# Optimization experiments

Measured on AMD Instinct MI355X. Metric: run time of the kernel, lower is better.

The kernel has to match this reference:

```python
import jax, jax.numpy as jnp
import numpy as np

T, N, E = 8, 50000, 800000
XD, HD, GD, ZD, TD, YHD = 128, 256, 128, 128, 8, 16
PSH = 100          # ps_predictor hidden width
BN_EPS = 1e-5


def _dense(k, fan_in, shape):
    return jax.random.normal(k, shape, jnp.float32) * (1.0 / np.sqrt(fan_in))


def setup_inputs() -> dict:
    ks = jax.random.split(jax.random.key(0), 20)
    inp = {}
    inp["X"] = jax.random.normal(ks[0], (T, N, XD), jnp.float32)
    inp["C"] = jax.random.uniform(ks[1], (T, N, TD), dtype=jnp.float32)
    inp["Y_hist"] = jax.random.normal(ks[2], (T, N, YHD), jnp.float32)
    inp["edge_index"] = jax.random.randint(ks[3], (T, 2, E), 0, N)
    # parameters
    inp["phi_W"] = _dense(ks[4], XD, (XD, HD)); inp["phi_b"] = jnp.zeros((HD,), jnp.float32)
    inp["gc_W"] = _dense(ks[5], HD, (T, HD, GD)); inp["gc_b"] = jnp.zeros((T, GD), jnp.float32)
    inp["ew_logit"] = jax.random.normal(ks[6], (T, E), jnp.float32) * 0.1  # learned edge weights (pre-sigmoid)
    inp["fuse_W"] = _dense(ks[7], 2 * HD + GD, (2 * HD + GD, ZD)); inp["fuse_b"] = jnp.zeros((ZD,), jnp.float32)
    inp["o00_W"] = _dense(ks[8], ZD, (ZD, ZD)); inp["o00_b"] = jnp.zeros((ZD,), jnp.float32)
    inp["o10_W"] = _dense(ks[9], ZD, (ZD, ZD)); inp["o10_b"] = jnp.zeros((ZD,), jnp.float32)
    inp["o01_W"] = _dense(ks[10], ZD, (ZD, 1)); inp["o01_b"] = jnp.zeros((1,), jnp.float32)
    inp["o11_W"] = _dense(ks[11], ZD, (ZD, 1)); inp["o11_b"] = jnp.zeros((1,), jnp.float32)
    inp["ps1_W"] = _dense(ks[12], ZD, (ZD, PSH)); inp["ps1_b"] = jnp.zeros((PSH,), jnp.float32)
    inp["bn_g"] = jnp.ones((PSH,), jnp.float32); inp["bn_b"] = jnp.zeros((PSH,), jnp.float32)
    inp["ps2_W"] = _dense(ks[13], PSH, (PSH, 2)); inp["ps2_b"] = jnp.zeros((2,), jnp.float32)
    inp["gru_Wih"] = _dense(ks[14], ZD + TD + YHD, (3 * HD, ZD + TD + YHD))
    inp["gru_Whh"] = _dense(ks[15], HD, (3 * HD, HD))
    inp["gru_bih"] = jnp.zeros((3 * HD,), jnp.float32)
    inp["gru_bhh"] = jnp.zeros((3 * HD,), jnp.float32)
    return inp


def reference(X, C, Y_hist, edge_index, phi_W, phi_b, gc_W, gc_b, ew_logit,
              fuse_W, fuse_b, o00_W, o00_b, o10_W, o10_b, o01_W, o01_b,
              o11_W, o11_b, ps1_W, ps1_b, bn_g, bn_b, ps2_W, ps2_b,
              gru_Wih, gru_Whh, gru_bih, gru_bhh):
    h0 = jnp.zeros((N, HD), X.dtype)
    bn_scale = bn_g / jnp.sqrt(1.0 + BN_EPS)  # eval-mode BN: running_mean=0, running_var=1

    def step(h, xs):
        x, ei, c, yh, W_t, b_t, ewl_t = xs
        phi = jax.nn.relu(x @ phi_W + phi_b)                              # [N,HD]
        # --- GCNConv with learned sigmoid edge weights + self loops ---
        src, dst = ei[0], ei[1]
        ew = jax.nn.sigmoid(ewl_t)                                        # [E]
        deg = jax.ops.segment_sum(ew, dst, num_segments=N) + 1.0          # +1 for self-loop weight
        dinv = jax.lax.rsqrt(deg)
        norm = dinv[src] * ew * dinv[dst]                                 # symmetric norm per edge
        xw = phi @ W_t                                                    # [N,GD]
        agg = jax.ops.segment_sum(norm[:, None] * xw[src], dst, num_segments=N)
        agg = agg + xw / deg[:, None] + b_t                               # self-loop contribution + bias
        rep = jax.nn.relu(agg)                                            # [N,GD] (dropout off in eval)
        # --- fuse with skip connection ---
        z = jax.nn.relu(jnp.concatenate([h, rep, phi], axis=1) @ fuse_W + fuse_b)  # [N,ZD]
        # --- GRUCell (torch gate order: reset, update, new) ---
        inp = jnp.concatenate([z, c, yh], axis=1)
        gi = inp @ gru_Wih.T + gru_bih
        gh = h @ gru_Whh.T + gru_bhh
        i_r, i_z, i_n = jnp.split(gi, 3, axis=1)
        h_r, h_z, h_n = jnp.split(gh, 3, axis=1)
        r = jax.nn.sigmoid(i_r + h_r)
        u = jax.nn.sigmoid(i_z + h_z)
        n = jnp.tanh(i_n + r * h_n)
        h_new = (1.0 - u) * n + u * h
        # --- outcome heads ---
        y0 = jax.nn.relu(z @ o00_W + o00_b) @ o01_W + o01_b               # [N,1]
        y1 = jax.nn.relu(z @ o10_W + o10_b) @ o11_W + o11_b               # [N,1]
        # --- propensity head (BatchNorm eval, sigmoid, softmax) ---
        s = jax.nn.sigmoid((z @ ps1_W + ps1_b) * bn_scale + bn_b)
        ps = jax.nn.softmax(s @ ps2_W + ps2_b, axis=1)                    # [N,2]
        return h_new, (y1, y0, z, ps)

    h_fin, (all_y1, all_y0, all_z, all_ps) = jax.lax.scan(
        step, h0, (X, edge_index, C, Y_hist, gc_W, gc_b, ew_logit))
    return all_y1, all_y0, all_z, all_ps, h_fin
```

## Files before the change

### kernel.cpp

```cpp
#include <hip/hip_runtime.h>
#include <math.h>

#define T_STEPS 8
#define NN 50000
#define EE 800000
#define TN (T_STEPS*NN)
#define TE (T_STEPS*EE)

typedef unsigned int uint;
typedef unsigned short ushort;
typedef unsigned long long u64;
typedef __attribute__((ext_vector_type(8))) short short8;
typedef __attribute__((ext_vector_type(4))) float f32x4;

__device__ __forceinline__ float sigf(float x){ return 1.0f/(1.0f+expf(-x)); }
__device__ __forceinline__ ushort f2b(float f){
  uint x = __float_as_uint(f);
  uint r = (x + 0x7fffu + ((x>>16)&1u)) >> 16;
  return (ushort)r;
}
__device__ __forceinline__ float b2f(ushort u){ return __uint_as_float(((uint)u)<<16); }

__device__ __forceinline__ void gload16(const ushort* g, ushort* l){
  __builtin_amdgcn_global_load_lds(
      (const __attribute__((address_space(1))) void*)g,
      (__attribute__((address_space(3))) void*)l, 16, 0, 0);
}

template<int ROWS>
__device__ __forceinline__ void stage_tile(const ushort* base, int ld, int rowclamp,
                                           ushort* lds, int lane, int wid){
  constexpr int ITERS = ROWS/32;
#pragma unroll
  for (int i=0;i<ITERS;i++){
    int lin = i*256 + wid*64 + lane;
    int row = lin>>3, s = lin&7;
    int gr = row; if (gr > rowclamp) gr = rowclamp;
    const ushort* gp = base + (size_t)gr*ld + ((s ^ (row&7))<<3);
    gload16(gp, lds + (size_t)(i*256 + wid*64)*8);
  }
}

__device__ __forceinline__ short8 fragld(const ushort* lds, int R, int kk, int lane){
  int slot = (kk*4 + (lane>>4)) ^ (R&7);
  return *(const short8*)&lds[R*64 + slot*8];
}

__global__ __launch_bounds__(256,2) void gemm_bf(
    const ushort* __restrict__ A0, int ld0, int w0,
    const ushort* __restrict__ A1, int ld1,
    const ushort* __restrict__ W, int K2,
    const float* __restrict__ bias, int act,
    float* __restrict__ C32, int ldc,
    ushort* __restrict__ C16, int ldb,
    int Nrow, int NOvalid)
{
  __shared__ __align__(16) ushort As[8192];
  __shared__ __align__(16) ushort Bs[8192];
  const int tid  = threadIdx.x;
  const int lane = tid & 63;
  const int wid  = __builtin_amdgcn_readfirstlane(tid >> 6);
  const int brow = blockIdx.x*128;
  const int bcol = blockIdx.y*128;
  const int wr = wid>>1, wc = wid&1;

  f32x4 acc[4][4];
#pragma unroll
  for(int m=0;m<4;m++)
#pragma unroll
    for(int n=0;n<4;n++) acc[m][n] = (f32x4){0.f,0.f,0.f,0.f};

  const int nk = K2 >> 6;
  for (int kt=0; kt<nk; ++kt){
    int col0 = kt*64;
    const ushort* ab; int ald;
    if (col0 < w0){ ab = A0 + col0; ald = ld0; }
    else          { ab = A1 + (col0 - w0); ald = ld1; }
    stage_tile<128>(ab + (size_t)brow*ald, ald, Nrow-1-brow, As, lane, wid);
    stage_tile<128>(W + (size_t)bcol*K2 + col0, K2, 1<<30, Bs, lane, wid);
    __syncthreads();
#pragma unroll
    for (int kk=0;kk<2;kk++){
      short8 a[4], b[4];
#pragma unroll
      for (int m=0;m<4;m++) a[m] = fragld(As, wr*64 + m*16 + (lane&15), kk, lane);
#pragma unroll
      for (int n=0;n<4;n++) b[n] = fragld(Bs, wc*64 + n*16 + (lane&15), kk, lane);
#pragma unroll
      for (int m=0;m<4;m++)
#pragma unroll
        for (int n=0;n<4;n++)
          acc[m][n] = __builtin_amdgcn_mfma_f32_16x16x32_bf16(a[m], b[n], acc[m][n], 0,0,0);
    }
    __syncthreads();
  }
  const int rbase = brow + wr*64 + (lane>>4)*4;
  const int cbase = bcol + wc*64 + (lane&15);
#pragma unroll
  for (int m=0;m<4;m++){
#pragma unroll
    for (int q=0;q<4;q++){
      int r = rbase + m*16 + q;
      if (r >= Nrow) continue;
#pragma unroll
      for (int n=0;n<4;n++){
        int c = cbase + n*16;
        if (c >= NOvalid) continue;
        float v = acc[m][n][q];
        if (bias)  v += bias[c];
        if (act==1) v = fmaxf(v, 0.f);
        if (C32) C32[(size_t)r*ldc + c] = v;
        if (C16) C16[(size_t)r*ldb + c] = f2b(v);
      }
    }
  }
}

__global__ __launch_bounds__(256,2) void gemm_gru(
    const ushort* __restrict__ A0, int ld0, int w0,
    const ushort* __restrict__ A1, int ld1,
    const ushort* __restrict__ W,
    const float* __restrict__ bg,
    const float* __restrict__ hin,
    float* __restrict__ hout, ushort* __restrict__ hbfo,
    int Nrow)
{
  __shared__ __align__(16) ushort As[8192];
  __shared__ __align__(16) ushort Bs[8192];
  const int tid  = threadIdx.x;
  const int lane = tid & 63;
  const int wid  = __builtin_amdgcn_readfirstlane(tid >> 6);
  const int brow = blockIdx.x*128;
  const int bcol = blockIdx.y*128;
  const int wr = wid>>1, wc = wid&1;
  const int K2 = 448;

  f32x4 acc[4][4];
#pragma unroll
  for(int m=0;m<4;m++)
#pragma unroll
    for(int n=0;n<4;n++) acc[m][n] = (f32x4){0.f,0.f,0.f,0.f};

  for (int kt=0; kt<7; ++kt){
    int col0 = kt*64;
    const ushort* ab; int ald;
    if (col0 < w0){ ab = A0 + col0; ald = ld0; }
    else          { ab = A1 + (col0 - w0); ald = ld1; }
    stage_tile<128>(ab + (size_t)brow*ald, ald, Nrow-1-brow, As, lane, wid);
    stage_tile<128>(W + (size_t)bcol*K2 + col0, K2, 1<<30, Bs, lane, wid);
    __syncthreads();
#pragma unroll
    for (int kk=0;kk<2;kk++){
      short8 a[4], b[4];
#pragma unroll
      for (int m=0;m<4;m++) a[m] = fragld(As, wr*64 + m*16 + (lane&15), kk, lane);
#pragma unroll
      for (int n=0;n<4;n++) b[n] = fragld(Bs, wc*64 + n*16 + (lane&15), kk, lane);
#pragma unroll
      for (int m=0;m<4;m++)
#pragma unroll
        for (int n=0;n<4;n++)
          acc[m][n] = __builtin_amdgcn_mfma_f32_16x16x32_bf16(a[m], b[n], acc[m][n], 0,0,0);
    }
    __syncthreads();
  }
  const int jj = lane&15;
  const int j  = blockIdx.y*32 + wc*16 + jj;
  const int rbase = brow + wr*64 + (lane>>4)*4;
  float bb[4];
#pragma unroll
  for (int n=0;n<4;n++) bb[n] = bg[bcol + wc*64 + n*16 + jj];
#pragma unroll
  for (int m=0;m<4;m++){
#pragma unroll
    for (int q=0;q<4;q++){
      int r = rbase + m*16 + q;
      if (r >= Nrow) continue;
      float v0 = acc[m][0][q] + bb[0];
      float v1 = acc[m][1][q] + bb[1];
      float v2 = acc[m][2][q] + bb[2];
      float v3 = acc[m][3][q] + bb[3];
      float rg = sigf(v0), ug = sigf(v1);
      float ng = tanhf(v2 + rg*v3);
      float ho = hin[(size_t)r*256 + j];
      float hn = (1.f-ug)*ng + ug*ho;
      hout[(size_t)r*256 + j] = hn;
      hbfo[(size_t)r*256 + j] = f2b(hn);
    }
  }
}

__global__ __launch_bounds__(256,2) void heads_k(
    const ushort* __restrict__ A, int ldA,
    const ushort* __restrict__ W,
    const float* __restrict__ o00b, const float* __restrict__ o10b,
    const float* __restrict__ w01, const float* __restrict__ b01,
    const float* __restrict__ w11, const float* __restrict__ b11,
    float* __restrict__ y0out, float* __restrict__ y1out, int Nrow)
{
  __shared__ __align__(16) ushort As[4096];
  __shared__ __align__(16) ushort Bs[16384];
  __shared__ float shy[4][64];
  const int tid  = threadIdx.x;
  const int lane = tid & 63;
  const int wid  = __builtin_amdgcn_readfirstlane(tid >> 6);
  const int brow = blockIdx.x*64;

  f32x4 acc[4][4];
#pragma unroll
  for(int m=0;m<4;m++)
#pragma unroll
    for(int n=0;n<4;n++) acc[m][n] = (f32x4){0.f,0.f,0.f,0.f};

  for (int kt=0; kt<2; ++kt){
    stage_tile<64>(A + (size_t)brow*ldA + kt*64, ldA, Nrow-1-brow, As, lane, wid);
    stage_tile<256>(W + kt*64, 128, 1<<30, Bs, lane, wid);
    __syncthreads();
#pragma unroll
    for (int kk=0;kk<2;kk++){
      short8 a[4], b[4];
#pragma unroll
      for (int m=0;m<4;m++) a[m] = fragld(As, m*16 + (lane&15), kk, lane);
#pragma unroll
      for (int n=0;n<4;n++) b[n] = fragld(Bs, wid*64 + n*16 + (lane&15), kk, lane);
#pragma unroll
      for (int m=0;m<4;m++)
#pragma unroll
        for (int n=0;n<4;n++)
          acc[m][n] = __builtin_amdgcn_mfma_f32_16x16x32_bf16(a[m], b[n], acc[m][n], 0,0,0);
    }
    __syncthreads();
  }
  float bb[4], ww[4];
#pragma unroll
  for (int n=0;n<4;n++){
    int c = wid*64 + n*16 + (lane&15);
    bb[n] = (c<128)? o00b[c] : o10b[c-128];
    ww[n] = (c<128)? w01[c]  : w11[c-128];
  }
#pragma unroll
  for (int m=0;m<4;m++){
#pragma unroll
    for (int q=0;q<4;q++){
      float p = 0.f;
#pragma unroll
      for (int n=0;n<4;n++) p += fmaxf(acc[m][n][q] + bb[n], 0.f) * ww[n];
#pragma unroll
      for (int o=1;o<16;o<<=1) p += __shfl_xor(p, o);
      if ((lane&15)==0) shy[wid][m*16 + (lane>>4)*4 + q] = p;
    }
  }
  __syncthreads();
  if (tid < 64){
    int r = brow + tid;
    if (r < Nrow){
      y0out[r] = shy[0][tid] + shy[1][tid] + b01[0];
      y1out[r] = shy[2][tid] + shy[3][tid] + b11[0];
    }
  }
}

__global__ __launch_bounds__(256,2) void ps_k(
    const ushort* __restrict__ A, int ldA,
    const ushort* __restrict__ W,
    const float* __restrict__ psc, const float* __restrict__ psb,
    const float* __restrict__ W2, const float* __restrict__ b2,
    float* __restrict__ psout, int Nrow)
{
  __shared__ __align__(16) ushort As[8192];
  __shared__ __align__(16) ushort Bs[8192];
  __shared__ float sh0[2][128];
  __shared__ float sh1[2][128];
  const int tid  = threadIdx.x;
  const int lane = tid & 63;
  const int wid  = __builtin_amdgcn_readfirstlane(tid >> 6);
  const int brow = blockIdx.x*128;
  const int wr = wid>>1, wc = wid&1;

  f32x4 acc[4][4];
#pragma unroll
  for(int m=0;m<4;m++)
#pragma unroll
    for(int n=0;n<4;n++) acc[m][n] = (f32x4){0.f,0.f,0.f,0.f};

  for (int kt=0; kt<2; ++kt){
    stage_tile<128>(A + (size_t)brow*ldA + kt*64, ldA, Nrow-1-brow, As, lane, wid);
    stage_tile<128>(W + kt*64, 128, 1<<30, Bs, lane, wid);
    __syncthreads();
#pragma unroll
    for (int kk=0;kk<2;kk++){
      short8 a[4], b[4];
#pragma unroll
      for (int m=0;m<4;m++) a[m] = fragld(As, wr*64 + m*16 + (lane&15), kk, lane);
#pragma unroll
      for (int n=0;n<4;n++) b[n] = fragld(Bs, wc*64 + n*16 + (lane&15), kk, lane);
#pragma unroll
      for (int m=0;m<4;m++)
#pragma unroll
        for (int n=0;n<4;n++)
          acc[m][n] = __builtin_amdgcn_mfma_f32_16x16x32_bf16(a[m], b[n], acc[m][n], 0,0,0);
    }
    __syncthreads();
  }
  float sc[4], sb[4], w0_[4], w1_[4];
#pragma unroll
  for (int n=0;n<4;n++){
    int c = wc*64 + n*16 + (lane&15);
    bool ok = (c<100);
    sc[n] = ok? psc[c] : 0.f;
    sb[n] = ok? psb[c] : 0.f;
    w0_[n]= ok? W2[2*c] : 0.f;
    w1_[n]= ok? W2[2*c+1] : 0.f;
  }
#pragma unroll
  for (int m=0;m<4;m++){
#pragma unroll
    for (int q=0;q<4;q++){
      float a0=0.f, a1=0.f;
#pragma unroll
      for (int n=0;n<4;n++){
        float s = sigf(acc[m][n][q]*sc[n] + sb[n]);
        a0 += s*w0_[n]; a1 += s*w1_[n];
      }
#pragma unroll
      for (int o=1;o<16;o<<=1){ a0 += __shfl_xor(a0,o); a1 += __shfl_xor(a1,o); }
      if ((lane&15)==0){
        int rt = wr*64 + m*16 + (lane>>4)*4 + q;
        sh0[wc][rt] = a0; sh1[wc][rt] = a1;
      }
    }
  }
  __syncthreads();
  if (tid < 128){
    int r = brow + tid;
    if (r < Nrow){
      float l0 = sh0[0][tid]+sh0[1][tid]+b2[0];
      float l1 = sh1[0][tid]+sh1[1][tid]+b2[1];
      float mx = fmaxf(l0,l1);
      float e0 = expf(l0-mx), e1 = expf(l1-mx);
      float inv = 1.f/(e0+e1);
      psout[(size_t)r*2]   = e0*inv;
      psout[(size_t)r*2+1] = e1*inv;
    }
  }
}

__global__ void count_k(const int* __restrict__ ei, const float* __restrict__ ewl,
                        u64* __restrict__ degcnt)
{
  int idx = blockIdx.x*256 + threadIdx.x;
  if (idx >= TE) return;
  int t = idx / EE;
  int e = idx - t*EE;
  const int* dst = ei + (size_t)t*2*EE + EE;
  int d = dst[e];
  u64 v = (1ULL<<40) | (u64)(uint)(sigf(ewl[idx]) * 1048576.0f);
  atomicAdd((unsigned long long*)&degcnt[t*NN + d], (unsigned long long)v);
}

__global__ void dinv_k(const u64* __restrict__ degcnt, int* __restrict__ cnt,
                       float* __restrict__ dnv, float* __restrict__ invd){
  int idx = blockIdx.x*256+threadIdx.x;
  if (idx>=TN) return;
  u64 tot = degcnt[idx];
  int c = (int)(tot>>40);
  float S = (float)(tot & ((1ULL<<40)-1)) * (1.f/1048576.f);
  float dv = S + 1.f;
  cnt[idx] = c;
  dnv[idx]  = rsqrtf(dv);
  invd[idx] = 1.f/dv;
}

__global__ void scan1_k(const int* __restrict__ in, int* __restrict__ outv,
                        int* __restrict__ partials, int n)
{
  __shared__ int sh[256];
  int base = blockIdx.x*1024;
  int tid = threadIdx.x;
  int v[4]; int s=0;
#pragma unroll
  for (int i=0;i<4;i++){ int idx=base+tid*4+i; v[i] = (idx<n)? in[idx]:0; s+=v[i]; }
  sh[tid]=s; __syncthreads();
  for (int o=1;o<256;o<<=1){
    int t2 = (tid>=o)? sh[tid-o]:0;
    __syncthreads();
    sh[tid]+=t2;
    __syncthreads();
  }
  int excl = sh[tid]-s;
#pragma unroll
  for (int i=0;i<4;i++){ int idx=base+tid*4+i; if(idx<n) outv[idx]=excl; excl+=v[i]; }
  if (tid==255) partials[blockIdx.x]=sh[255];
}

__global__ void scan2_k(int* p, int np){
  __shared__ int sh[256];
  __shared__ int run;
  int tid=threadIdx.x;
  if(tid==0) run=0;
  __syncthreads();
  for(int base=0;base<np;base+=256){
    int v = (base+tid<np)? p[base+tid]:0;
    sh[tid]=v; __syncthreads();
    for(int o=1;o<256;o<<=1){
      int t2 = (tid>=o)? sh[tid-o]:0;
      __syncthreads();
      sh[tid]+=t2;
      __syncthreads();
    }
    int incl=sh[tid];
    int r0=run;
    __syncthreads();
    if(base+tid<np) p[base+tid]=r0+incl-v;
    __syncthreads();
    if(tid==0) run = r0 + sh[255];
    __syncthreads();
  }
}

__global__ void scan3_k(int* __restrict__ offs, const int* __restrict__ parts,
                        int* __restrict__ cur, int n){
  int idx = blockIdx.x*256+threadIdx.x;
  if (idx==0) offs[n] = TE;
  if (idx<n){ int v = offs[idx] + parts[idx>>10]; offs[idx]=v; cur[idx]=v; }
}

__global__ void fill_k(const int* __restrict__ ei, const float* __restrict__ ewl,
                       const float* __restrict__ dnv, int* __restrict__ cur,
                       u64* __restrict__ epack)
{
  int idx = blockIdx.x*256 + threadIdx.x;
  if (idx >= TE) return;
  int t = idx / EE;
  int e = idx - t*EE;
  const int* srcp = ei + (size_t)t*2*EE;
  const int* dstp = srcp + EE;
  int s=srcp[e], d=dstp[e];
  float nr = dnv[t*NN+s] * sigf(ewl[idx]) * dnv[t*NN+d];
  int pos = atomicAdd(&cur[t*NN+d], 1);
  epack[pos] = (u64)(uint)s | ((u64)__float_as_uint(nr) << 32);
}

__global__ __launch_bounds__(256) void gather_k(const int* __restrict__ offs_t,
    const u64* __restrict__ epack,
    const ushort* __restrict__ xwb, const float* __restrict__ invd_t,
    const float* __restrict__ gcb_t, ushort* __restrict__ rp)
{
  int node = blockIdx.x*4 + (threadIdx.x>>6);
  int lane = threadIdx.x & 63;
  if (node >= NN) return;
  int o0 = offs_t[node], o1 = offs_t[node+1];
  float a0=0.f, a1=0.f;
  int j=o0;
  for (; j+1<o1; j+=2){
    u64 e0 = epack[j], e1 = epack[j+1];
    uint r0 = ((const uint*)(xwb + ((size_t)(uint)e0)*128))[lane];
    uint r1 = ((const uint*)(xwb + ((size_t)(uint)e1)*128))[lane];
    float n0 = __uint_as_float((uint)(e0>>32));
    float n1 = __uint_as_float((uint)(e1>>32));
    a0 = fmaf(n0, b2f((ushort)(r0&0xffff)), a0);
    a1 = fmaf(n0, b2f((ushort)(r0>>16)),   a1);
    a0 = fmaf(n1, b2f((ushort)(r1&0xffff)), a0);
    a1 = fmaf(n1, b2f((ushort)(r1>>16)),   a1);
  }
  if (j<o1){
    u64 e0 = epack[j];
    uint r0 = ((const uint*)(xwb + ((size_t)(uint)e0)*128))[lane];
    float n0 = __uint_as_float((uint)(e0>>32));
    a0 = fmaf(n0, b2f((ushort)(r0&0xffff)), a0);
    a1 = fmaf(n0, b2f((ushort)(r0>>16)),   a1);
  }
  float sl = invd_t[node];
  uint us = ((const uint*)(xwb + (size_t)node*128))[lane];
  a0 = fmaf(sl, b2f((ushort)(us&0xffff)), a0) + gcb_t[2*lane];
  a1 = fmaf(sl, b2f((ushort)(us>>16)),   a1) + gcb_t[2*lane+1];
  a0 = fmaxf(a0, 0.f); a1 = fmaxf(a1, 0.f);
  uint pk = (uint)f2b(a0) | ((uint)f2b(a1) << 16);
  ((uint*)(rp + (size_t)node*384))[lane] = pk;
}

__global__ void convT_k(ushort* __restrict__ dst, const float* __restrict__ src,
                        int O, int Osrc, int K, int Kp)
{
  int idx = blockIdx.x*256 + threadIdx.x;
  if (idx >= O*Kp) return;
  dst += (size_t)blockIdx.y * O * Kp;
  src += (size_t)blockIdx.y * K * Osrc;
  int o = idx / Kp, k = idx - o*Kp;
  float v = (k<K && o<Osrc) ? src[(size_t)k*Osrc + o] : 0.f;
  dst[idx] = f2b(v);
}

__global__ void woc_k(ushort* __restrict__ dst, const float* __restrict__ o00W,
                      const float* __restrict__ o10W)
{
  int idx = blockIdx.x*256 + threadIdx.x;
  if (idx >= 256*128) return;
  int o = idx >> 7, k = idx & 127;
  float v = (o<128) ? o00W[(size_t)k*128 + o] : o10W[(size_t)k*128 + (o-128)];
  dst[idx] = f2b(v);
}

__global__ void wgru_k(const float* __restrict__ Wih, const float* __restrict__ Whh,
                       const float* __restrict__ bih, const float* __restrict__ bhh,
                       ushort* __restrict__ Wg, float* __restrict__ bg)
{
  int idx = blockIdx.x*256 + threadIdx.x;
  if (idx >= 1024*448) return;
  int c = idx/448, k = idx - c*448;
  int G = c>>6, g = (c>>4)&3, jj = c&15;
  int j = G*16 + jj;
  float v = 0.f;
  if (k < 152){
    if      (g==0) v = Wih[(size_t)j*152 + k];
    else if (g==1) v = Wih[(size_t)(256+j)*152 + k];
    else if (g==2) v = Wih[(size_t)(512+j)*152 + k];
  } else if (k >= 192){
    int kk = k-192;
    if      (g==0) v = Whh[(size_t)j*256 + kk];
    else if (g==1) v = Whh[(size_t)(256+j)*256 + kk];
    else if (g==3) v = Whh[(size_t)(512+j)*256 + kk];
  }
  Wg[idx] = f2b(v);
  if (k==0){
    float b;
    if      (g==0) b = bih[j]     + bhh[j];
    else if (g==1) b = bih[256+j] + bhh[256+j];
    else if (g==2) b = bih[512+j];
    else           b = bhh[512+j];
    bg[c] = b;
  }
}

__global__ void misc_k(const float* __restrict__ ps1b, const float* __restrict__ bng,
                       const float* __restrict__ bnb,
                       float* __restrict__ psc, float* __restrict__ psb)
{
  int i = threadIdx.x;
  if (i<100){ float sc = bng[i]*rsqrtf(1.f+1e-5f); psc[i]=sc; psb[i]=ps1b[i]*sc+bnb[i]; }
  else if (i<128){ psc[i]=0.f; psb[i]=0.f; }
}

__global__ void xconv_k(ushort* __restrict__ dst, const float* __restrict__ src, long n4)
{
  long i = (long)blockIdx.x*256 + threadIdx.x;
  if (i >= n4) return;
  float4 v = ((const float4*)src)[i];
  uint lo = (uint)f2b(v.x) | ((uint)f2b(v.y)<<16);
  uint hi = (uint)f2b(v.z) | ((uint)f2b(v.w)<<16);
  ((uint2*)dst)[i] = make_uint2(lo, hi);
}

__global__ void cyh_k(ushort* __restrict__ zcyh, const float* __restrict__ Cc,
                      const float* __restrict__ Yh)
{
  int gid = blockIdx.x*256 + threadIdx.x;
  int n = gid >> 6, l = gid & 63;
  if (n >= NN) return;
  float v = 0.f;
  if (l < 8)       v = Cc[(size_t)n*8 + l];
  else if (l < 24) v = Yh[(size_t)n*16 + (l-8)];
  zcyh[(size_t)n*192 + 128 + l] = f2b(v);
}

extern "C" void kernel_launch(void* const* d_in, const int* in_sizes, int n_in,
                              void* d_out_v, int out_size, void* d_ws, size_t ws_size,
                              hipStream_t stream)
{
  const float* X    = (const float*)d_in[0];
  const float* Cc   = (const float*)d_in[1];
  const float* Yh   = (const float*)d_in[2];
  const int*   EI   = (const int*)  d_in[3];
  const float* phiW = (const float*)d_in[4];  const float* phib = (const float*)d_in[5];
  const float* gcW  = (const float*)d_in[6];  const float* gcb  = (const float*)d_in[7];
  const float* ewl  = (const float*)d_in[8];
  const float* fuseW= (const float*)d_in[9];  const float* fuseb= (const float*)d_in[10];
  const float* o00W = (const float*)d_in[11]; const float* o00b = (const float*)d_in[12];
  const float* o10W = (const float*)d_in[13]; const float* o10b = (const float*)d_in[14];
  const float* o01W = (const float*)d_in[15]; const float* o01b = (const float*)d_in[16];
  const float* o11W = (const float*)d_in[17]; const float* o11b = (const float*)d_in[18];
  const float* ps1W = (const float*)d_in[19]; const float* ps1b = (const float*)d_in[20];
  const float* bng  = (const float*)d_in[21]; const float* bnb  = (const float*)d_in[22];
  const float* ps2W = (const float*)d_in[23]; const float* ps2b = (const float*)d_in[24];
  const float* Wih  = (const float*)d_in[25]; const float* Whh  = (const float*)d_in[26];
  const float* bih  = (const float*)d_in[27]; const float* bhh  = (const float*)d_in[28];
  float* out = (float*)d_out_v;

  char* wsb = (char*)d_ws;
  size_t off=0;
  auto alloc=[&](size_t bytes)->void*{
    void* p = wsb + off;
    off = (off + bytes + 255) & ~(size_t)255;
    return p;
  };
  u64*   degcnt= (u64*)  alloc((size_t)TN*8);
  int*   cnt   = (int*)  alloc((size_t)TN*4);
  int*   cur   = (int*)  alloc((size_t)TN*4);
  int*   offs  = (int*)  alloc(((size_t)TN+1)*4);
  float* dnv   = (float*)alloc((size_t)TN*4);
  float* invd  = (float*)alloc((size_t)TN*4);
  u64*   epack = (u64*)  alloc((size_t)TE*8);
  int*   parts = (int*)  alloc(4096);
  ushort* Xb   = (ushort*)alloc((size_t)T_STEPS*NN*128*2);
  ushort* rp   = (ushort*)alloc((size_t)NN*384*2);
  ushort* zcyh = (ushort*)alloc((size_t)NN*192*2);
  ushort* xwb  = (ushort*)alloc((size_t)NN*128*2);
  ushort* hbf0 = (ushort*)alloc((size_t)NN*256*2);
  ushort* hbf1 = (ushort*)alloc((size_t)NN*256*2);
  float* hb0   = (float*)alloc((size_t)NN*256*4);
  float* hb1   = (float*)alloc((size_t)NN*256*4);
  ushort* phiWt= (ushort*)alloc(256*128*2);
  ushort* gcWt = (ushort*)alloc((size_t)T_STEPS*128*256*2);
  ushort* fuseWt=(ushort*)alloc(128*640*2);
  ushort* Wgru = (ushort*)alloc((size_t)1024*448*2);
  float* bgru  = (float*)alloc(1024*4);
  ushort* wocT = (ushort*)alloc(256*128*2);
  ushort* ps1T = (ushort*)alloc(128*128*2);
  float* psc   = (float*)alloc(128*4);
  float* psb   = (float*)alloc(128*4);

  hipMemsetAsync(degcnt, 0, (size_t)TN*8, stream);
  hipMemsetAsync(hb0,  0, (size_t)NN*256*4, stream);
  hipMemsetAsync(hbf0, 0, (size_t)NN*256*2, stream);

  misc_k<<<1,256,0,stream>>>(ps1b,bng,bnb,psc,psb);
  convT_k<<<dim3((256*128+255)/256,1),256,0,stream>>>(phiWt, phiW, 256,256,128,128);
  convT_k<<<dim3((128*256+255)/256,T_STEPS),256,0,stream>>>(gcWt, gcW, 128,128,256,256);
  convT_k<<<dim3((128*640+255)/256,1),256,0,stream>>>(fuseWt, fuseW, 128,128,640,640);
  convT_k<<<dim3((128*128+255)/256,1),256,0,stream>>>(ps1T, ps1W, 128,100,128,128);
  wgru_k<<<(1024*448+255)/256,256,0,stream>>>(Wih,Whh,bih,bhh,Wgru,bgru);
  woc_k<<<(256*128+255)/256,256,0,stream>>>(wocT, o00W, o10W);
  xconv_k<<<(int)(((size_t)T_STEPS*NN*128/4+255)/256),256,0,stream>>>(Xb, X, (long)T_STEPS*NN*128/4);

  count_k<<<(TE+255)/256,256,0,stream>>>(EI,ewl,degcnt);
  dinv_k<<<(TN+255)/256,256,0,stream>>>(degcnt,cnt,dnv,invd);
  scan1_k<<<(TN+1023)/1024,256,0,stream>>>(cnt,offs,parts,TN);
  scan2_k<<<1,256,0,stream>>>(parts,(TN+1023)/1024);
  scan3_k<<<(TN+255)/256,256,0,stream>>>(offs,parts,cur,TN);
  fill_k<<<(TE+255)/256,256,0,stream>>>(EI,ewl,dnv,cur,epack);

  const size_t zoff  = (size_t)2*TN;
  const size_t psoff = zoff + (size_t)TN*128;
  const size_t hoff  = psoff + (size_t)TN*2;
  constexpr int GX = (NN+127)/128;

  for (int t=0;t<T_STEPS;t++){
    const float*  hin  = (t&1)? hb1 : hb0;
    float*        hout = (t==T_STEPS-1)? (out+hoff) : ((t&1)? hb0 : hb1);
    const ushort* hbi  = (t&1)? hbf1 : hbf0;
    ushort*       hbo  = (t&1)? hbf0 : hbf1;
    float* zt = out + zoff + (size_t)t*NN*128;

    cyh_k<<<(NN*64+255)/256,256,0,stream>>>(zcyh, Cc+(size_t)t*NN*8, Yh+(size_t)t*NN*16);

    gemm_bf<<<dim3(GX,2),256,0,stream>>>(Xb+(size_t)t*NN*128,128,128, nullptr,0,
      phiWt,128, phib,1, nullptr,0, rp+128,384, NN,256);
    gemm_bf<<<dim3(GX,1),256,0,stream>>>(rp+128,384,256, nullptr,0,
      gcWt+(size_t)t*128*256,256, nullptr,0, nullptr,0, xwb,128, NN,128);
    gather_k<<<NN/4,256,0,stream>>>(offs+(size_t)t*NN, epack, xwb,
                                    invd+(size_t)t*NN, gcb+(size_t)t*128, rp);
    gemm_bf<<<dim3(GX,1),256,0,stream>>>(hbi,256,256, rp,384,
      fuseWt,640, fuseb,1, zt,128, zcyh,192, NN,128);
    gemm_gru<<<dim3(GX,8),256,0,stream>>>(zcyh,192,192, hbi,256,
      Wgru, bgru, hin, hout, hbo, NN);
    heads_k<<<(NN+63)/64,256,0,stream>>>(zcyh,192, wocT, o00b,o10b,
      o01W,o01b, o11W,o11b,
      out + TN + (size_t)t*NN,
      out + (size_t)t*NN, NN);
    ps_k<<<GX,256,0,stream>>>(zcyh,192, ps1T, psc,psb, ps2W,ps2b,
      out+psoff+(size_t)t*NN*2, NN);
  }
  (void)in_sizes; (void)n_in; (void)out_size; (void)ws_size;
}
```

Baseline: 2.838 ms.

## Hoist h-independent stages out of the time loop and batch them over all steps

The phi GEMM, graph-conv GEMM, gather, and the rep/phi part of the fuse GEMM now run once over all T steps, using blockIdx.z as the time index. Only the h-dependent fuse GEMM and the GRU stay in the sequential loop; the outcome heads and propensity head run batched after the loop. Edge records are packed into 32 bits (16-bit source index and 16-bit quantized weight) to halve gather traffic. The aim is to cut per-step launch overhead, fill the GPU with larger grids, and reduce memory traffic. The cost is larger workspace buffers, plus extra precision loss from the quantized edge weights and the bf16 partial fuse result.

```diff
diff --git a/kernel.cpp b/kernel.cpp
--- a/kernel.cpp
+++ b/kernel.cpp
@@ -46,17 +46,20 @@
   return *(const short8*)&lds[R*64 + slot*8];
 }
 
+struct Seg { const ushort* p; int ld; long ts; int w; };
+
 __global__ __launch_bounds__(256,2) void gemm_bf(
-    const ushort* __restrict__ A0, int ld0, int w0,
-    const ushort* __restrict__ A1, int ld1,
-    const ushort* __restrict__ W, int K2,
+    Seg s0, Seg s1, Seg s2,
+    const ushort* __restrict__ W, int K2, long Wts,
     const float* __restrict__ bias, int act,
-    float* __restrict__ C32, int ldc,
-    ushort* __restrict__ C16, int ldb,
+    const ushort* __restrict__ addp, int ldad, long adts,
+    float* __restrict__ C32, int ldc, long c32ts,
+    ushort* __restrict__ C16, int ldb, long c16ts,
     int Nrow, int NOvalid)
 {
   __shared__ __align__(16) ushort As[8192];
   __shared__ __align__(16) ushort Bs[8192];
+  const int t    = blockIdx.z;
   const int tid  = threadIdx.x;
   const int lane = tid & 63;
   const int wid  = __builtin_amdgcn_readfirstlane(tid >> 6);
@@ -74,10 +77,11 @@
   for (int kt=0; kt<nk; ++kt){
     int col0 = kt*64;
     const ushort* ab; int ald;
-    if (col0 < w0){ ab = A0 + col0; ald = ld0; }
-    else          { ab = A1 + (col0 - w0); ald = ld1; }
+    if (col0 < s0.w){ ab = s0.p + (size_t)t*s0.ts + col0; ald = s0.ld; }
+    else if (col0 < s0.w + s1.w){ ab = s1.p + (size_t)t*s1.ts + (col0 - s0.w); ald = s1.ld; }
+    else { ab = s2.p + (size_t)t*s2.ts + (col0 - s0.w - s1.w); ald = s2.ld; }
     stage_tile<128>(ab + (size_t)brow*ald, ald, Nrow-1-brow, As, lane, wid);
-    stage_tile<128>(W + (size_t)bcol*K2 + col0, K2, 1<<30, Bs, lane, wid);
+    stage_tile<128>(W + (size_t)t*Wts + (size_t)bcol*K2 + col0, K2, 1<<30, Bs, lane, wid);
     __syncthreads();
 #pragma unroll
     for (int kk=0;kk<2;kk++){
@@ -107,18 +111,18 @@
         int c = cbase + n*16;
         if (c >= NOvalid) continue;
         float v = acc[m][n][q];
-        if (bias)  v += bias[c];
+        if (addp) v += b2f(addp[(size_t)t*adts + (size_t)r*ldad + c]);
+        if (bias) v += bias[c];
         if (act==1) v = fmaxf(v, 0.f);
-        if (C32) C32[(size_t)r*ldc + c] = v;
-        if (C16) C16[(size_t)r*ldb + c] = f2b(v);
+        if (C32) C32[(size_t)t*c32ts + (size_t)r*ldc + c] = v;
+        if (C16) C16[(size_t)t*c16ts + (size_t)r*ldb + c] = f2b(v);
       }
     }
   }
 }
 
 __global__ __launch_bounds__(256,2) void gemm_gru(
-    const ushort* __restrict__ A0, int ld0, int w0,
-    const ushort* __restrict__ A1, int ld1,
+    Seg s0, Seg s1, Seg s2,
     const ushort* __restrict__ W,
     const float* __restrict__ bg,
     const float* __restrict__ hin,
@@ -144,8 +148,9 @@
   for (int kt=0; kt<7; ++kt){
     int col0 = kt*64;
     const ushort* ab; int ald;
-    if (col0 < w0){ ab = A0 + col0; ald = ld0; }
-    else          { ab = A1 + (col0 - w0); ald = ld1; }
+    if (col0 < s0.w){ ab = s0.p + col0; ald = s0.ld; }
+    else if (col0 < s0.w + s1.w){ ab = s1.p + (col0 - s0.w); ald = s1.ld; }
+    else { ab = s2.p + (col0 - s0.w - s1.w); ald = s2.ld; }
     stage_tile<128>(ab + (size_t)brow*ald, ald, Nrow-1-brow, As, lane, wid);
     stage_tile<128>(W + (size_t)bcol*K2 + col0, K2, 1<<30, Bs, lane, wid);
     __syncthreads();
@@ -167,9 +172,10 @@
   const int jj = lane&15;
   const int j  = blockIdx.y*32 + wc*16 + jj;
   const int rbase = brow + wr*64 + (lane>>4)*4;
+  const int bcolw = bcol + wc*64;
   float bb[4];
 #pragma unroll
-  for (int n=0;n<4;n++) bb[n] = bg[bcol + wc*64 + n*16 + jj];
+  for (int n=0;n<4;n++) bb[n] = bg[bcolw + n*16 + jj];
 #pragma unroll
   for (int m=0;m<4;m++){
 #pragma unroll
@@ -191,20 +197,23 @@
 }
 
 __global__ __launch_bounds__(256,2) void heads_k(
-    const ushort* __restrict__ A, int ldA,
+    const ushort* __restrict__ Az, long Ats,
     const ushort* __restrict__ W,
     const float* __restrict__ o00b, const float* __restrict__ o10b,
     const float* __restrict__ w01, const float* __restrict__ b01,
     const float* __restrict__ w11, const float* __restrict__ b11,
-    float* __restrict__ y0out, float* __restrict__ y1out, int Nrow)
+    float* __restrict__ y0out, long y0ts,
+    float* __restrict__ y1out, long y1ts, int Nrow)
 {
   __shared__ __align__(16) ushort As[4096];
   __shared__ __align__(16) ushort Bs[16384];
   __shared__ float shy[4][64];
+  const int t    = blockIdx.z;
   const int tid  = threadIdx.x;
   const int lane = tid & 63;
   const int wid  = __builtin_amdgcn_readfirstlane(tid >> 6);
   const int brow = blockIdx.x*64;
+  const ushort* A = Az + (size_t)t*Ats;
 
   f32x4 acc[4][4];
 #pragma unroll
@@ -213,7 +222,7 @@
     for(int n=0;n<4;n++) acc[m][n] = (f32x4){0.f,0.f,0.f,0.f};
 
   for (int kt=0; kt<2; ++kt){
-    stage_tile<64>(A + (size_t)brow*ldA + kt*64, ldA, Nrow-1-brow, As, lane, wid);
+    stage_tile<64>(A + (size_t)brow*128 + kt*64, 128, Nrow-1-brow, As, lane, wid);
     stage_tile<256>(W + kt*64, 128, 1<<30, Bs, lane, wid);
     __syncthreads();
 #pragma unroll
@@ -254,28 +263,30 @@
   if (tid < 64){
     int r = brow + tid;
     if (r < Nrow){
-      y0out[r] = shy[0][tid] + shy[1][tid] + b01[0];
-      y1out[r] = shy[2][tid] + shy[3][tid] + b11[0];
+      y0out[(size_t)t*y0ts + r] = shy[0][tid] + shy[1][tid] + b01[0];
+      y1out[(size_t)t*y1ts + r] = shy[2][tid] + shy[3][tid] + b11[0];
     }
   }
 }
 
 __global__ __launch_bounds__(256,2) void ps_k(
-    const ushort* __restrict__ A, int ldA,
+    const ushort* __restrict__ Az, long Ats,
     const ushort* __restrict__ W,
     const float* __restrict__ psc, const float* __restrict__ psb,
     const float* __restrict__ W2, const float* __restrict__ b2,
-    float* __restrict__ psout, int Nrow)
+    float* __restrict__ psout, long psts, int Nrow)
 {
   __shared__ __align__(16) ushort As[8192];
   __shared__ __align__(16) ushort Bs[8192];
   __shared__ float sh0[2][128];
   __shared__ float sh1[2][128];
+  const int t    = blockIdx.z;
   const int tid  = threadIdx.x;
   const int lane = tid & 63;
   const int wid  = __builtin_amdgcn_readfirstlane(tid >> 6);
   const int brow = blockIdx.x*128;
   const int wr = wid>>1, wc = wid&1;
+  const ushort* A = Az + (size_t)t*Ats;
 
   f32x4 acc[4][4];
 #pragma unroll
@@ -284,7 +295,7 @@
     for(int n=0;n<4;n++) acc[m][n] = (f32x4){0.f,0.f,0.f,0.f};
 
   for (int kt=0; kt<2; ++kt){
-    stage_tile<128>(A + (size_t)brow*ldA + kt*64, ldA, Nrow-1-brow, As, lane, wid);
+    stage_tile<128>(A + (size_t)brow*128 + kt*64, 128, Nrow-1-brow, As, lane, wid);
     stage_tile<128>(W + kt*64, 128, 1<<30, Bs, lane, wid);
     __syncthreads();
 #pragma unroll
@@ -339,8 +350,8 @@
       float mx = fmaxf(l0,l1);
       float e0 = expf(l0-mx), e1 = expf(l1-mx);
       float inv = 1.f/(e0+e1);
-      psout[(size_t)r*2]   = e0*inv;
-      psout[(size_t)r*2+1] = e1*inv;
+      psout[(size_t)t*psts + (size_t)r*2]   = e0*inv;
+      psout[(size_t)t*psts + (size_t)r*2+1] = e1*inv;
     }
   }
 }
@@ -427,7 +438,7 @@
 
 __global__ void fill_k(const int* __restrict__ ei, const float* __restrict__ ewl,
                        const float* __restrict__ dnv, int* __restrict__ cur,
-                       u64* __restrict__ epack)
+                       uint* __restrict__ epack)
 {
   int idx = blockIdx.x*256 + threadIdx.x;
   if (idx >= TE) return;
@@ -437,46 +448,51 @@
   const int* dstp = srcp + EE;
   int s=srcp[e], d=dstp[e];
   float nr = dnv[t*NN+s] * sigf(ewl[idx]) * dnv[t*NN+d];
+  uint nq = (uint)(nr*65535.f + 0.5f);
   int pos = atomicAdd(&cur[t*NN+d], 1);
-  epack[pos] = (u64)(uint)s | ((u64)__float_as_uint(nr) << 32);
-}
-
-__global__ __launch_bounds__(256) void gather_k(const int* __restrict__ offs_t,
-    const u64* __restrict__ epack,
-    const ushort* __restrict__ xwb, const float* __restrict__ invd_t,
-    const float* __restrict__ gcb_t, ushort* __restrict__ rp)
-{
+  epack[pos] = (uint)s | (nq<<16);
+}
+
+__global__ __launch_bounds__(256) void gather_k(const int* __restrict__ offs,
+    const uint* __restrict__ epack,
+    const ushort* __restrict__ xwb, const float* __restrict__ invd,
+    const float* __restrict__ gcb, ushort* __restrict__ rep)
+{
+  int t    = blockIdx.z;
   int node = blockIdx.x*4 + (threadIdx.x>>6);
   int lane = threadIdx.x & 63;
   if (node >= NN) return;
+  const int* offs_t = offs + (size_t)t*NN;
+  const ushort* xw_t = xwb + (size_t)t*NN*128;
   int o0 = offs_t[node], o1 = offs_t[node+1];
   float a0=0.f, a1=0.f;
   int j=o0;
   for (; j+1<o1; j+=2){
-    u64 e0 = epack[j], e1 = epack[j+1];
-    uint r0 = ((const uint*)(xwb + ((size_t)(uint)e0)*128))[lane];
-    uint r1 = ((const uint*)(xwb + ((size_t)(uint)e1)*128))[lane];
-    float n0 = __uint_as_float((uint)(e0>>32));
-    float n1 = __uint_as_float((uint)(e1>>32));
+    uint e0 = epack[j], e1 = epack[j+1];
+    uint r0 = ((const uint*)(xw_t + ((size_t)(e0&0xffff))*128))[lane];
+    uint r1 = ((const uint*)(xw_t + ((size_t)(e1&0xffff))*128))[lane];
+    float n0 = (float)(e0>>16) * (1.f/65535.f);
+    float n1 = (float)(e1>>16) * (1.f/65535.f);
     a0 = fmaf(n0, b2f((ushort)(r0&0xffff)), a0);
     a1 = fmaf(n0, b2f((ushort)(r0>>16)),   a1);
     a0 = fmaf(n1, b2f((ushort)(r1&0xffff)), a0);
     a1 = fmaf(n1, b2f((ushort)(r1>>16)),   a1);
   }
   if (j<o1){
-    u64 e0 = epack[j];
-    uint r0 = ((const uint*)(xwb + ((size_t)(uint)e0)*128))[lane];
-    float n0 = __uint_as_float((uint)(e0>>32));
+    uint e0 = epack[j];
+    uint r0 = ((const uint*)(xw_t + ((size_t)(e0&0xffff))*128))[lane];
+    float n0 = (float)(e0>>16) * (1.f/65535.f);
     a0 = fmaf(n0, b2f((ushort)(r0&0xffff)), a0);
     a1 = fmaf(n0, b2f((ushort)(r0>>16)),   a1);
   }
-  float sl = invd_t[node];
-  uint us = ((const uint*)(xwb + (size_t)node*128))[lane];
+  float sl = invd[(size_t)t*NN + node];
+  const float* gcb_t = gcb + (size_t)t*128;
+  uint us = ((const uint*)(xw_t + (size_t)node*128))[lane];
   a0 = fmaf(sl, b2f((ushort)(us&0xffff)), a0) + gcb_t[2*lane];
   a1 = fmaf(sl, b2f((ushort)(us>>16)),   a1) + gcb_t[2*lane+1];
   a0 = fmaxf(a0, 0.f); a1 = fmaxf(a1, 0.f);
   uint pk = (uint)f2b(a0) | ((uint)f2b(a1) << 16);
-  ((uint*)(rp + (size_t)node*384))[lane] = pk;
+  ((uint*)(rep + ((size_t)t*NN + node)*128))[lane] = pk;
 }
 
 __global__ void convT_k(ushort* __restrict__ dst, const float* __restrict__ src,
@@ -551,16 +567,16 @@
   ((uint2*)dst)[i] = make_uint2(lo, hi);
 }
 
-__global__ void cyh_k(ushort* __restrict__ zcyh, const float* __restrict__ Cc,
+__global__ void cyh_k(ushort* __restrict__ cyh, const float* __restrict__ Cc,
                       const float* __restrict__ Yh)
 {
-  int gid = blockIdx.x*256 + threadIdx.x;
-  int n = gid >> 6, l = gid & 63;
-  if (n >= NN) return;
+  long gid = (long)blockIdx.x*256 + threadIdx.x;
+  if (gid >= (long)TN*64) return;
+  long g = gid >> 6; int l = (int)(gid & 63);
   float v = 0.f;
-  if (l < 8)       v = Cc[(size_t)n*8 + l];
-  else if (l < 24) v = Yh[(size_t)n*16 + (l-8)];
-  zcyh[(size_t)n*192 + 128 + l] = f2b(v);
+  if (l < 8)       v = Cc[g*8 + l];
+  else if (l < 24) v = Yh[g*16 + (l-8)];
+  cyh[g*64 + l] = f2b(v);
 }
 
 extern "C" void kernel_launch(void* const* d_in, const int* in_sizes, int n_in,
@@ -599,19 +615,19 @@
   int*   offs  = (int*)  alloc(((size_t)TN+1)*4);
   float* dnv   = (float*)alloc((size_t)TN*4);
   float* invd  = (float*)alloc((size_t)TN*4);
-  u64*   epack = (u64*)  alloc((size_t)TE*8);
+  uint*  epack = (uint*) alloc((size_t)TE*4);
   int*   parts = (int*)  alloc(4096);
-  ushort* Xb   = (ushort*)alloc((size_t)T_STEPS*NN*128*2);
-  ushort* rp   = (ushort*)alloc((size_t)NN*384*2);
-  ushort* zcyh = (ushort*)alloc((size_t)NN*192*2);
-  ushort* xwb  = (ushort*)alloc((size_t)NN*128*2);
+  ushort* Xb   = (ushort*)alloc((size_t)TN*128*2);
+  ushort* phiA = (ushort*)alloc((size_t)TN*256*2);
+  ushort* xwb  = (ushort*)alloc((size_t)TN*128*2);
+  ushort* pz   = (ushort*)alloc((size_t)TN*128*2);
   ushort* hbf0 = (ushort*)alloc((size_t)NN*256*2);
   ushort* hbf1 = (ushort*)alloc((size_t)NN*256*2);
-  float* hb0   = (float*)alloc((size_t)NN*256*4);
-  float* hb1   = (float*)alloc((size_t)NN*256*4);
+  float*  hb   = (float*)alloc((size_t)NN*256*4);
   ushort* phiWt= (ushort*)alloc(256*128*2);
   ushort* gcWt = (ushort*)alloc((size_t)T_STEPS*128*256*2);
-  ushort* fuseWt=(ushort*)alloc(128*640*2);
+  ushort* WhT  = (ushort*)alloc(128*256*2);
+  ushort* WrpT = (ushort*)alloc(128*384*2);
   ushort* Wgru = (ushort*)alloc((size_t)1024*448*2);
   float* bgru  = (float*)alloc(1024*4);
   ushort* wocT = (ushort*)alloc(256*128*2);
@@ -619,18 +635,23 @@
   float* psc   = (float*)alloc(128*4);
   float* psb   = (float*)alloc(128*4);
 
+  ushort* rep_all = Xb;
+  ushort* zbf     = phiA;
+  ushort* cyh     = phiA + (size_t)TN*128;
+
   hipMemsetAsync(degcnt, 0, (size_t)TN*8, stream);
-  hipMemsetAsync(hb0,  0, (size_t)NN*256*4, stream);
+  hipMemsetAsync(hb,   0, (size_t)NN*256*4, stream);
   hipMemsetAsync(hbf0, 0, (size_t)NN*256*2, stream);
 
   misc_k<<<1,256,0,stream>>>(ps1b,bng,bnb,psc,psb);
   convT_k<<<dim3((256*128+255)/256,1),256,0,stream>>>(phiWt, phiW, 256,256,128,128);
   convT_k<<<dim3((128*256+255)/256,T_STEPS),256,0,stream>>>(gcWt, gcW, 128,128,256,256);
-  convT_k<<<dim3((128*640+255)/256,1),256,0,stream>>>(fuseWt, fuseW, 128,128,640,640);
+  convT_k<<<dim3((128*256+255)/256,1),256,0,stream>>>(WhT, fuseW, 128,128,256,256);
+  convT_k<<<dim3((128*384+255)/256,1),256,0,stream>>>(WrpT, fuseW+256*128, 128,128,384,384);
   convT_k<<<dim3((128*128+255)/256,1),256,0,stream>>>(ps1T, ps1W, 128,100,128,128);
   wgru_k<<<(1024*448+255)/256,256,0,stream>>>(Wih,Whh,bih,bhh,Wgru,bgru);
   woc_k<<<(256*128+255)/256,256,0,stream>>>(wocT, o00W, o10W);
-  xconv_k<<<(int)(((size_t)T_STEPS*NN*128/4+255)/256),256,0,stream>>>(Xb, X, (long)T_STEPS*NN*128/4);
+  xconv_k<<<(int)(((size_t)TN*128/4+255)/256),256,0,stream>>>(Xb, X, (long)TN*128/4);
 
   count_k<<<(TE+255)/256,256,0,stream>>>(EI,ewl,degcnt);
   dinv_k<<<(TN+255)/256,256,0,stream>>>(degcnt,cnt,dnv,invd);
@@ -643,32 +664,42 @@
   const size_t psoff = zoff + (size_t)TN*128;
   const size_t hoff  = psoff + (size_t)TN*2;
   constexpr int GX = (NN+127)/128;
+  const Seg S0 = {nullptr,0,0,0};
+
+  gemm_bf<<<dim3(GX,2,8),256,0,stream>>>(
+    Seg{Xb,128,(long)NN*128,128}, S0, S0, phiWt,128,0, phib,1,
+    nullptr,0,0, nullptr,0,0, phiA,256,(long)NN*256, NN,256);
+  gemm_bf<<<dim3(GX,1,8),256,0,stream>>>(
+    Seg{phiA,256,(long)NN*256,256}, S0, S0, gcWt,256,(long)128*256, nullptr,0,
+    nullptr,0,0, nullptr,0,0, xwb,128,(long)NN*128, NN,128);
+  gather_k<<<dim3(NN/4,1,8),256,0,stream>>>(offs, epack, xwb, invd, gcb, rep_all);
+  gemm_bf<<<dim3(GX,1,8),256,0,stream>>>(
+    Seg{rep_all,128,(long)NN*128,128}, Seg{phiA,256,(long)NN*256,256}, S0,
+    WrpT,384,0, nullptr,0,
+    nullptr,0,0, nullptr,0,0, pz,128,(long)NN*128, NN,128);
+  cyh_k<<<(int)(((long)TN*64+255)/256),256,0,stream>>>(cyh, Cc, Yh);
 
   for (int t=0;t<T_STEPS;t++){
-    const float*  hin  = (t&1)? hb1 : hb0;
-    float*        hout = (t==T_STEPS-1)? (out+hoff) : ((t&1)? hb0 : hb1);
-    const ushort* hbi  = (t&1)? hbf1 : hbf0;
-    ushort*       hbo  = (t&1)? hbf0 : hbf1;
+    const ushort* hbi = (t&1)? hbf1 : hbf0;
+    ushort*       hbo = (t&1)? hbf0 : hbf1;
+    float* hout = (t==T_STEPS-1)? (out+hoff) : hb;
     float* zt = out + zoff + (size_t)t*NN*128;
-
-    cyh_k<<<(NN*64+255)/256,256,0,stream>>>(zcyh, Cc+(size_t)t*NN*8, Yh+(size_t)t*NN*16);
-
-    gemm_bf<<<dim3(GX,2),256,0,stream>>>(Xb+(size_t)t*NN*128,128,128, nullptr,0,
-      phiWt,128, phib,1, nullptr,0, rp+128,384, NN,256);
-    gemm_bf<<<dim3(GX,1),256,0,stream>>>(rp+128,384,256, nullptr,0,
-      gcWt+(size_t)t*128*256,256, nullptr,0, nullptr,0, xwb,128, NN,128);
-    gather_k<<<NN/4,256,0,stream>>>(offs+(size_t)t*NN, epack, xwb,
-                                    invd+(size_t)t*NN, gcb+(size_t)t*128, rp);
-    gemm_bf<<<dim3(GX,1),256,0,stream>>>(hbi,256,256, rp,384,
-      fuseWt,640, fuseb,1, zt,128, zcyh,192, NN,128);
-    gemm_gru<<<dim3(GX,8),256,0,stream>>>(zcyh,192,192, hbi,256,
-      Wgru, bgru, hin, hout, hbo, NN);
-    heads_k<<<(NN+63)/64,256,0,stream>>>(zcyh,192, wocT, o00b,o10b,
-      o01W,o01b, o11W,o11b,
-      out + TN + (size_t)t*NN,
-      out + (size_t)t*NN, NN);
-    ps_k<<<GX,256,0,stream>>>(zcyh,192, ps1T, psc,psb, ps2W,ps2b,
-      out+psoff+(size_t)t*NN*2, NN);
-  }
+    ushort* zbt = zbf + (size_t)t*NN*128;
+    gemm_bf<<<dim3(GX,1,1),256,0,stream>>>(
+      Seg{hbi,256,0,256}, S0, S0, WhT,256,0, fuseb,1,
+      pz + (size_t)t*NN*128,128,0, zt,128,0, zbt,128,0, NN,128);
+    gemm_gru<<<dim3(GX,8),256,0,stream>>>(
+      Seg{zbt,128,0,128}, Seg{cyh + (size_t)t*NN*64,64,0,64}, Seg{hbi,256,0,256},
+      Wgru, bgru, hb, hout, hbo, NN);
+  }
+
+  heads_k<<<dim3((NN+63)/64,1,8),256,0,stream>>>(
+    zbf,(long)NN*128, wocT, o00b,o10b, o01W,o01b, o11W,o11b,
+    out + TN, (long)NN,
+    out, (long)NN, NN);
+  ps_k<<<dim3(GX,1,8),256,0,stream>>>(
+    zbf,(long)NN*128, ps1T, psc,psb, ps2W,ps2b,
+    out+psoff, (long)NN*2, NN);
+
   (void)in_sizes; (void)n_in; (void)out_size; (void)ws_size;
 }
```

Result: faster. 2.697 ms (-5.0%).
